# Kernel tuning notes

Measured on AMD Instinct MI355X. Metric: run time of the kernel, lower is better.

Reference implementation:

```python
import jax, jax.numpy as jnp
import numpy as np

N = 2_000_000
FEAT = 128
S = 8192


def setup_inputs() -> dict:
    key = jax.random.key(0)
    k1, k2, k3, k4, k5 = jax.random.split(key, 5)
    x = jax.random.normal(k1, (N, FEAT), dtype=jnp.float32)
    subst_ids = jax.random.randint(k2, (N,), 0, S, dtype=jnp.int32)
    W1 = jax.random.normal(k3, (FEAT, 64), dtype=jnp.float32) * (1.0 / np.sqrt(FEAT))
    b1 = jax.random.normal(k4, (64,), dtype=jnp.float32) * 0.01
    w2 = jax.random.normal(k5, (64, 1), dtype=jnp.float32) * (1.0 / 8.0)
    return {"x": x, "subst_ids": subst_ids, "num_segments": S,
            "W1": W1, "b1": b1, "w2": w2}


def reference(x, subst_ids, num_segments, W1, b1, w2):
    # Segment mean over substructure ids (fused segment_sum + count).
    seg_sum = jax.ops.segment_sum(x, subst_ids, num_segments=num_segments)  # [S, F]
    counts = jax.ops.segment_sum(jnp.ones((x.shape[0],), x.dtype), subst_ids,
                                 num_segments=num_segments)                 # [S]
    means = seg_sum / jnp.maximum(counts, 1.0)[:, None]                     # [S, F]
    # Tiny attention MLP: Linear -> tanh -> Linear(no bias).
    scores = jnp.tanh(means @ W1 + b1) @ w2                                 # [S, 1]
    subst_attn = jax.nn.softmax(scores, axis=0)                             # [S, 1]
    # Scatter per-substructure attention back to each atom.
    atom_attn = subst_attn[subst_ids, 0]                                    # [N]
    return atom_attn[:, None]                                               # [N, 1]
```

## Files before the change

### kernel.cpp

```cpp
#include <hip/hip_runtime.h>
#include <math.h>

#define FEAT 128
#define SEG 8192
#define HID 64
#define CAP 512

typedef float f32x4 __attribute__((ext_vector_type(4)));
typedef int   i32x4 __attribute__((ext_vector_type(4)));

__global__ void scatter_kernel(const int* __restrict__ ids, int* __restrict__ cursor,
                               int* __restrict__ perm, int n) {
    const int tid = blockIdx.x * blockDim.x + threadIdx.x;
    const int stride = gridDim.x * blockDim.x;
    const int nv = n >> 2;
    for (int i = tid; i < nv; i += stride) {
        const i32x4 v = __builtin_nontemporal_load(
            reinterpret_cast<const i32x4*>(ids + i * 4));
        const int b = i * 4;
        int s0 = atomicAdd(&cursor[v.x], 1);
        int s1 = atomicAdd(&cursor[v.y], 1);
        int s2 = atomicAdd(&cursor[v.z], 1);
        int s3 = atomicAdd(&cursor[v.w], 1);
        if (s0 < CAP) perm[(v.x << 9) + s0] = b;
        if (s1 < CAP) perm[(v.y << 9) + s1] = b + 1;
        if (s2 < CAP) perm[(v.z << 9) + s2] = b + 2;
        if (s3 < CAP) perm[(v.w << 9) + s3] = b + 3;
    }
    for (int i = nv * 4 + tid; i < n; i += stride) {
        const int s = ids[i];
        const int sl = atomicAdd(&cursor[s], 1);
        if (sl < CAP) perm[(s << 9) + sl] = i;
    }
}

__global__ __launch_bounds__(256) void seg_reduce_mlp(
    const float* __restrict__ x, const int* __restrict__ perm, const int* __restrict__ cursor,
    const float* __restrict__ W1, const float* __restrict__ b1,
    const float* __restrict__ w2, float* __restrict__ scores) {
    const int s = blockIdx.x;
    const int cnt = min(cursor[s], CAP);
    const int t = threadIdx.x;
    const int grp = t >> 5;
    const unsigned lnoff = (t & 31) << 2;

    __shared__ int sperm[CAP];
    __shared__ float ssum[8][128];
    __shared__ float smean[128];

    const int nc4 = (cnt + 3) >> 2;
    const i32x4* pb = reinterpret_cast<const i32x4*>(perm + (s << 9));
    i32x4* sp4 = reinterpret_cast<i32x4*>(sperm);
    for (int j = t; j < nc4; j += 256) sp4[j] = pb[j];
    __syncthreads();

    f32x4 acc = (f32x4)(0.f);
    const int m = cnt;
    int r = grp;
    for (; r + 56 < m; r += 64) {
        const f32x4 v0 = __builtin_nontemporal_load(
            reinterpret_cast<const f32x4*>(x + (((unsigned)sperm[r]      << 7) + lnoff)));
        const f32x4 v1 = __builtin_nontemporal_load(
            reinterpret_cast<const f32x4*>(x + (((unsigned)sperm[r + 8]  << 7) + lnoff)));
        const f32x4 v2 = __builtin_nontemporal_load(
            reinterpret_cast<const f32x4*>(x + (((unsigned)sperm[r + 16] << 7) + lnoff)));
        const f32x4 v3 = __builtin_nontemporal_load(
            reinterpret_cast<const f32x4*>(x + (((unsigned)sperm[r + 24] << 7) + lnoff)));
        const f32x4 v4 = __builtin_nontemporal_load(
            reinterpret_cast<const f32x4*>(x + (((unsigned)sperm[r + 32] << 7) + lnoff)));
        const f32x4 v5 = __builtin_nontemporal_load(
            reinterpret_cast<const f32x4*>(x + (((unsigned)sperm[r + 40] << 7) + lnoff)));
        const f32x4 v6 = __builtin_nontemporal_load(
            reinterpret_cast<const f32x4*>(x + (((unsigned)sperm[r + 48] << 7) + lnoff)));
        const f32x4 v7 = __builtin_nontemporal_load(
            reinterpret_cast<const f32x4*>(x + (((unsigned)sperm[r + 56] << 7) + lnoff)));
        acc += ((v0 + v1) + (v2 + v3)) + ((v4 + v5) + (v6 + v7));
    }
    for (; r + 24 < m; r += 32) {
        const f32x4 v0 = __builtin_nontemporal_load(
            reinterpret_cast<const f32x4*>(x + (((unsigned)sperm[r]      << 7) + lnoff)));
        const f32x4 v1 = __builtin_nontemporal_load(
            reinterpret_cast<const f32x4*>(x + (((unsigned)sperm[r + 8]  << 7) + lnoff)));
        const f32x4 v2 = __builtin_nontemporal_load(
            reinterpret_cast<const f32x4*>(x + (((unsigned)sperm[r + 16] << 7) + lnoff)));
        const f32x4 v3 = __builtin_nontemporal_load(
            reinterpret_cast<const f32x4*>(x + (((unsigned)sperm[r + 24] << 7) + lnoff)));
        acc += (v0 + v1) + (v2 + v3);
    }
    for (; r < m; r += 8) {
        acc += __builtin_nontemporal_load(
            reinterpret_cast<const f32x4*>(x + (((unsigned)sperm[r] << 7) + lnoff)));
    }

    *reinterpret_cast<f32x4*>(&ssum[grp][lnoff]) = acc;
    __syncthreads();

    if (t < 128) {
        float tot = 0.f;
        #pragma unroll
        for (int g = 0; g < 8; ++g) tot += ssum[g][t];
        smean[t] = tot / fmaxf((float)cnt, 1.0f);
    }
    __syncthreads();

    if (t < 64) {
        float h = b1[t];
        #pragma unroll
        for (int ff = 0; ff < FEAT; ++ff) h = fmaf(smean[ff], W1[ff * HID + t], h);
        float v = tanhf(h) * w2[t];
        #pragma unroll
        for (int off = 32; off; off >>= 1) v += __shfl_down(v, off, 64);
        if (t == 0) scores[s] = v;
    }
}

__global__ void softmax8192(const float* __restrict__ scores, float* __restrict__ attn) {
    __shared__ float sval[SEG];
    __shared__ float red[16];
    __shared__ float red2[16];
    const int T = blockDim.x;
    const int t = threadIdx.x;
    const int wid = t >> 6, lane = t & 63;

    float m = -1e30f;
    for (int i = t; i < SEG; i += T) {
        const float v = scores[i];
        sval[i] = v;
        m = fmaxf(m, v);
    }
    #pragma unroll
    for (int off = 32; off; off >>= 1) m = fmaxf(m, __shfl_xor(m, off, 64));
    if (lane == 0) red[wid] = m;
    __syncthreads();
    if (t == 0) {
        float mm = red[0];
        for (int i = 1; i < 16; ++i) mm = fmaxf(mm, red[i]);
        red[0] = mm;
    }
    __syncthreads();
    m = red[0];

    float sum = 0.0f;
    for (int i = t; i < SEG; i += T) sum += expf(sval[i] - m);
    #pragma unroll
    for (int off = 32; off; off >>= 1) sum += __shfl_xor(sum, off, 64);
    if (lane == 0) red2[wid] = sum;
    __syncthreads();
    if (t == 0) {
        float ss = 0.0f;
        for (int i = 0; i < 16; ++i) ss += red2[i];
        red2[0] = ss;
    }
    __syncthreads();
    const float invZ = 1.0f / red2[0];
    for (int i = t; i < SEG; i += T) attn[i] = expf(sval[i] - m) * invZ;
}

__global__ void gather_attn(const int* __restrict__ ids, const float* __restrict__ attn,
                            float* __restrict__ out, int n) {
    const int i = blockIdx.x * blockDim.x + threadIdx.x;
    const int i4 = i * 4;
    if (i4 + 3 < n) {
        const i32x4 id4 = __builtin_nontemporal_load(
            reinterpret_cast<const i32x4*>(ids + i4));
        f32x4 o;
        o.x = attn[id4.x];
        o.y = attn[id4.y];
        o.z = attn[id4.z];
        o.w = attn[id4.w];
        __builtin_nontemporal_store(o, reinterpret_cast<f32x4*>(out + i4));
    } else {
        for (int k = i4; k < n; ++k) out[k] = attn[ids[k]];
    }
}

extern "C" void kernel_launch(void* const* d_in, const int* in_sizes, int n_in,
                              void* d_out, int out_size, void* d_ws, size_t ws_size,
                              hipStream_t stream) {
    const float* x   = (const float*)d_in[0];
    const int*   ids = (const int*)d_in[1];
    const float* W1  = (const float*)d_in[3];
    const float* b1  = (const float*)d_in[4];
    const float* w2  = (const float*)d_in[5];
    float* out = (float*)d_out;
    const int n = in_sizes[1];

    char* ws = (char*)d_ws;
    int*   cursor = (int*)ws;
    float* scores = (float*)(cursor + SEG);
    float* attn   = scores + SEG;
    int*   perm   = (int*)(attn + SEG);

    hipMemsetAsync(cursor, 0, SEG * sizeof(int), stream);

    scatter_kernel<<<2048, 256, 0, stream>>>(ids, cursor, perm, n);
    seg_reduce_mlp<<<SEG, 256, 0, stream>>>(x, perm, cursor, W1, b1, w2, scores);
    softmax8192<<<1, 1024, 0, stream>>>(scores, attn);

    const int nv = (n + 3) / 4;
    gather_attn<<<(nv + 255) / 256, 256, 0, stream>>>(ids, attn, out, n);
}
```

Baseline: 257.9 us.

## Map one wavefront per segment in reduce+MLP, replacing LDS with shuffles

The segment reduction moves from one 256-thread block per segment to one 64-lane wavefront per segment, four segments per block. The permutation indices are loaded into registers and broadcast with lane shuffles instead of being staged in shared memory, and the final mean and MLP are done with cross-lane shuffles instead of LDS reductions and __syncthreads. This removes block-level barriers and LDS traffic and lets each segment proceed independently, at the cost of fewer in-flight loads per segment (two rows per step instead of eight) and more shuffle instructions.

```diff
diff --git a/kernel.cpp b/kernel.cpp
--- a/kernel.cpp
+++ b/kernel.cpp
@@ -38,80 +38,87 @@
     const float* __restrict__ x, const int* __restrict__ perm, const int* __restrict__ cursor,
     const float* __restrict__ W1, const float* __restrict__ b1,
     const float* __restrict__ w2, float* __restrict__ scores) {
-    const int s = blockIdx.x;
+    const int s = (blockIdx.x * blockDim.x + threadIdx.x) >> 6;
+    const int l = threadIdx.x & 63;
+    const int half = l >> 5;
+    const unsigned q = (l & 31) << 2;
+
     const int cnt = min(cursor[s], CAP);
-    const int t = threadIdx.x;
-    const int grp = t >> 5;
-    const unsigned lnoff = (t & 31) << 2;
-
-    __shared__ int sperm[CAP];
-    __shared__ float ssum[8][128];
-    __shared__ float smean[128];
-
-    const int nc4 = (cnt + 3) >> 2;
-    const i32x4* pb = reinterpret_cast<const i32x4*>(perm + (s << 9));
-    i32x4* sp4 = reinterpret_cast<i32x4*>(sperm);
-    for (int j = t; j < nc4; j += 256) sp4[j] = pb[j];
-    __syncthreads();
+    const int base = s << 9;
 
     f32x4 acc = (f32x4)(0.f);
-    const int m = cnt;
-    int r = grp;
-    for (; r + 56 < m; r += 64) {
-        const f32x4 v0 = __builtin_nontemporal_load(
-            reinterpret_cast<const f32x4*>(x + (((unsigned)sperm[r]      << 7) + lnoff)));
-        const f32x4 v1 = __builtin_nontemporal_load(
-            reinterpret_cast<const f32x4*>(x + (((unsigned)sperm[r + 8]  << 7) + lnoff)));
-        const f32x4 v2 = __builtin_nontemporal_load(
-            reinterpret_cast<const f32x4*>(x + (((unsigned)sperm[r + 16] << 7) + lnoff)));
-        const f32x4 v3 = __builtin_nontemporal_load(
-            reinterpret_cast<const f32x4*>(x + (((unsigned)sperm[r + 24] << 7) + lnoff)));
-        const f32x4 v4 = __builtin_nontemporal_load(
-            reinterpret_cast<const f32x4*>(x + (((unsigned)sperm[r + 32] << 7) + lnoff)));
-        const f32x4 v5 = __builtin_nontemporal_load(
-            reinterpret_cast<const f32x4*>(x + (((unsigned)sperm[r + 40] << 7) + lnoff)));
-        const f32x4 v6 = __builtin_nontemporal_load(
-            reinterpret_cast<const f32x4*>(x + (((unsigned)sperm[r + 48] << 7) + lnoff)));
-        const f32x4 v7 = __builtin_nontemporal_load(
-            reinterpret_cast<const f32x4*>(x + (((unsigned)sperm[r + 56] << 7) + lnoff)));
-        acc += ((v0 + v1) + (v2 + v3)) + ((v4 + v5) + (v6 + v7));
-    }
-    for (; r + 24 < m; r += 32) {
-        const f32x4 v0 = __builtin_nontemporal_load(
-            reinterpret_cast<const f32x4*>(x + (((unsigned)sperm[r]      << 7) + lnoff)));
-        const f32x4 v1 = __builtin_nontemporal_load(
-            reinterpret_cast<const f32x4*>(x + (((unsigned)sperm[r + 8]  << 7) + lnoff)));
-        const f32x4 v2 = __builtin_nontemporal_load(
-            reinterpret_cast<const f32x4*>(x + (((unsigned)sperm[r + 16] << 7) + lnoff)));
-        const f32x4 v3 = __builtin_nontemporal_load(
-            reinterpret_cast<const f32x4*>(x + (((unsigned)sperm[r + 24] << 7) + lnoff)));
-        acc += (v0 + v1) + (v2 + v3);
-    }
-    for (; r < m; r += 8) {
-        acc += __builtin_nontemporal_load(
-            reinterpret_cast<const f32x4*>(x + (((unsigned)sperm[r] << 7) + lnoff)));
-    }
-
-    *reinterpret_cast<f32x4*>(&ssum[grp][lnoff]) = acc;
-    __syncthreads();
-
-    if (t < 128) {
-        float tot = 0.f;
+
+    int chunk = 0;
+    for (; chunk + 64 <= cnt; chunk += 64) {
+        const int my = perm[base + chunk + l];
         #pragma unroll
-        for (int g = 0; g < 8; ++g) tot += ssum[g][t];
-        smean[t] = tot / fmaxf((float)cnt, 1.0f);
-    }
-    __syncthreads();
-
-    if (t < 64) {
-        float h = b1[t];
-        #pragma unroll
-        for (int ff = 0; ff < FEAT; ++ff) h = fmaf(smean[ff], W1[ff * HID + t], h);
-        float v = tanhf(h) * w2[t];
-        #pragma unroll
-        for (int off = 32; off; off >>= 1) v += __shfl_down(v, off, 64);
-        if (t == 0) scores[s] = v;
-    }
+        for (int st = 0; st < 32; st += 8) {
+            const int r0 = __shfl(my, 2 * (st + 0) + half, 64);
+            const int r1 = __shfl(my, 2 * (st + 1) + half, 64);
+            const int r2 = __shfl(my, 2 * (st + 2) + half, 64);
+            const int r3 = __shfl(my, 2 * (st + 3) + half, 64);
+            const int r4 = __shfl(my, 2 * (st + 4) + half, 64);
+            const int r5 = __shfl(my, 2 * (st + 5) + half, 64);
+            const int r6 = __shfl(my, 2 * (st + 6) + half, 64);
+            const int r7 = __shfl(my, 2 * (st + 7) + half, 64);
+            const f32x4 v0 = __builtin_nontemporal_load(
+                reinterpret_cast<const f32x4*>(x + (((unsigned)r0 << 7) + q)));
+            const f32x4 v1 = __builtin_nontemporal_load(
+                reinterpret_cast<const f32x4*>(x + (((unsigned)r1 << 7) + q)));
+            const f32x4 v2 = __builtin_nontemporal_load(
+                reinterpret_cast<const f32x4*>(x + (((unsigned)r2 << 7) + q)));
+            const f32x4 v3 = __builtin_nontemporal_load(
+                reinterpret_cast<const f32x4*>(x + (((unsigned)r3 << 7) + q)));
+            const f32x4 v4 = __builtin_nontemporal_load(
+                reinterpret_cast<const f32x4*>(x + (((unsigned)r4 << 7) + q)));
+            const f32x4 v5 = __builtin_nontemporal_load(
+                reinterpret_cast<const f32x4*>(x + (((unsigned)r5 << 7) + q)));
+            const f32x4 v6 = __builtin_nontemporal_load(
+                reinterpret_cast<const f32x4*>(x + (((unsigned)r6 << 7) + q)));
+            const f32x4 v7 = __builtin_nontemporal_load(
+                reinterpret_cast<const f32x4*>(x + (((unsigned)r7 << 7) + q)));
+            acc += ((v0 + v1) + (v2 + v3)) + ((v4 + v5) + (v6 + v7));
+        }
+    }
+    if (chunk < cnt) {
+        const int rem = cnt - chunk;
+        const int my = (l < rem) ? perm[base + chunk + l] : 0;
+        const int steps = (rem + 1) >> 1;
+        #pragma unroll 4
+        for (int st = 0; st < steps; ++st) {
+            const int idx = 2 * st + half;
+            const int row = __shfl(my, idx, 64);
+            if (idx < rem) {
+                acc += __builtin_nontemporal_load(
+                    reinterpret_cast<const f32x4*>(x + (((unsigned)row << 7) + q)));
+            }
+        }
+    }
+
+    acc.x += __shfl_xor(acc.x, 32, 64);
+    acc.y += __shfl_xor(acc.y, 32, 64);
+    acc.z += __shfl_xor(acc.z, 32, 64);
+    acc.w += __shfl_xor(acc.w, 32, 64);
+
+    const float inv = 1.0f / fmaxf((float)cnt, 1.0f);
+    acc *= inv;
+
+    float h = b1[l];
+    #pragma unroll
+    for (int qq = 0; qq < 32; ++qq) {
+        const float m0 = __shfl(acc.x, qq, 64);
+        const float m1 = __shfl(acc.y, qq, 64);
+        const float m2 = __shfl(acc.z, qq, 64);
+        const float m3 = __shfl(acc.w, qq, 64);
+        h = fmaf(m0, W1[(4 * qq + 0) * HID + l], h);
+        h = fmaf(m1, W1[(4 * qq + 1) * HID + l], h);
+        h = fmaf(m2, W1[(4 * qq + 2) * HID + l], h);
+        h = fmaf(m3, W1[(4 * qq + 3) * HID + l], h);
+    }
+    float v = tanhf(h) * w2[l];
+    #pragma unroll
+    for (int off = 32; off; off >>= 1) v += __shfl_down(v, off, 64);
+    if (l == 0) scores[s] = v;
 }
 
 __global__ void softmax8192(const float* __restrict__ scores, float* __restrict__ attn) {
@@ -194,7 +201,7 @@
     hipMemsetAsync(cursor, 0, SEG * sizeof(int), stream);
 
     scatter_kernel<<<2048, 256, 0, stream>>>(ids, cursor, perm, n);
-    seg_reduce_mlp<<<SEG, 256, 0, stream>>>(x, perm, cursor, W1, b1, w2, scores);
+    seg_reduce_mlp<<<SEG / 4, 256, 0, stream>>>(x, perm, cursor, W1, b1, w2, scores);
     softmax8192<<<1, 1024, 0, stream>>>(scores, attn);
 
     const int nv = (n + 3) / 4;
```

After: 269.9 us. +4.7%, slower.
